# Kernel tuning notes

Measured on AMD Instinct MI355X. Metric: run time of the kernel, lower is better.

The kernel has to match this reference:

```python
import jax, jax.numpy as jnp
import numpy as np

EPS = 1e-5

def layer_norm(x, w, b):
    mu = x.mean(-1, keepdims=True)
    var = x.var(-1, keepdims=True)
    return (x - mu) / jnp.sqrt(var + EPS) * w + b

def s5_forward(u, Lambda_re, Lambda_im, B_re, B_im, C_re, C_im, D, log_step):
    # u: [B, L, H]; diagonal S5 SSM with P complex states, ZOH discretization.
    Lam = (Lambda_re + 1j * Lambda_im).astype(jnp.complex64)          # [P]
    dt = jnp.exp(log_step).astype(jnp.complex64)                       # [P]
    Lam_bar = jnp.exp(Lam * dt)                                        # [P]
    Bc = (B_re + 1j * B_im).astype(jnp.complex64)                      # [P, H]
    B_bar = ((Lam_bar - 1.0) / Lam)[:, None] * Bc                      # [P, H]
    Bu = jnp.einsum('blh,ph->blp', u.astype(jnp.complex64), B_bar)     # [B, L, P]
    A = jnp.broadcast_to(Lam_bar, Bu.shape)                            # [B, L, P]

    def binop(e1, e2):
        a1, b1 = e1
        a2, b2 = e2
        return (a2 * a1, a2 * b1 + b2)

    _, xs = jax.lax.associative_scan(binop, (A, Bu), axis=1)           # [B, L, P]
    Cc = (C_re + 1j * C_im).astype(jnp.complex64)                      # [H, P]
    y = 2.0 * jnp.einsum('blp,hp->blh', xs, Cc).real + D * u           # [B, L, H]
    return y

def setup_inputs() -> dict:
    key = jax.random.key(0)
    ks = jax.random.split(key, 12)
    B, L, H, P = 4, 4096, 512, 512
    x = jax.random.normal(ks[0], (B, L, H), jnp.float32)
    # SSM params (HiPPO-like flavor: negative real part, spread imaginary part)
    Lambda_re = -(0.5 * jax.random.uniform(ks[1], (P,), jnp.float32) + 0.1)
    Lambda_im = jnp.pi * jnp.arange(P, dtype=jnp.float32)
    B_re = jax.random.normal(ks[2], (P, H), jnp.float32) / np.sqrt(2.0 * H)
    B_im = jax.random.normal(ks[3], (P, H), jnp.float32) / np.sqrt(2.0 * H)
    C_re = jax.random.normal(ks[4], (H, P), jnp.float32) / np.sqrt(P)
    C_im = jax.random.normal(ks[5], (H, P), jnp.float32) / np.sqrt(P)
    D = jax.random.normal(ks[6], (H,), jnp.float32)
    log_step = jax.random.uniform(ks[7], (P,), jnp.float32,
                                  minval=np.log(1e-3), maxval=np.log(1e-1))
    ln1_w = jnp.ones((H,), jnp.float32); ln1_b = jnp.zeros((H,), jnp.float32)
    ln2_w = jnp.ones((H,), jnp.float32); ln2_b = jnp.zeros((H,), jnp.float32)
    W_enc = jax.random.normal(ks[8], (2 * H, H), jnp.float32) / np.sqrt(H)
    W_dec = jax.random.normal(ks[9], (H, H), jnp.float32) / np.sqrt(H)
    return {"x": x, "ln1_w": ln1_w, "ln1_b": ln1_b,
            "Lambda_re": Lambda_re, "Lambda_im": Lambda_im,
            "B_re": B_re, "B_im": B_im, "C_re": C_re, "C_im": C_im,
            "D": D, "log_step": log_step,
            "ln2_w": ln2_w, "ln2_b": ln2_b, "W_enc": W_enc, "W_dec": W_dec}

def reference(x, ln1_w, ln1_b, Lambda_re, Lambda_im, B_re, B_im, C_re, C_im,
              D, log_step, ln2_w, ln2_b, W_enc, W_dec):
    fx = layer_norm(x, ln1_w, ln1_b)
    res = fx
    u = s5_forward(fx, Lambda_re, Lambda_im, B_re, B_im, C_re, C_im, D, log_step)
    h = jax.nn.gelu(u, approximate=False) + res  # eval mode: dropout = identity
    fx2 = layer_norm(h, ln2_w, ln2_b)
    e = fx2 @ W_enc.T                              # [B, L, 2H]
    a, g = jnp.split(e, 2, axis=-1)
    ff = a * jax.nn.gelu(g, approximate=False)     # GEGLU
    out = ff @ W_dec.T + fx2
    return out
```

## Files before the change

### kernel.cpp

```cpp
#include <hip/hip_runtime.h>
#include <math.h>

#define Bz 4
#define Lz 4096
#define Hz 512
#define Pz 512
#define Nz (Bz*Lz)
#define CL 64
#define NC (Lz/CL)
#define CS (Bz*NC*Pz)
#define EPSf 1e-5f

typedef unsigned short u16;
typedef unsigned int   u32;
typedef __attribute__((ext_vector_type(8))) short bf16x8;
typedef __attribute__((ext_vector_type(8))) short short8v;
typedef __attribute__((ext_vector_type(4))) short short4v;
typedef __attribute__((ext_vector_type(4))) float f32x4;

__device__ __forceinline__ float gelu_exact(float x){
    return 0.5f * x * (1.0f + erff(x * 0.70710678118654752f));
}
__device__ __forceinline__ u16 f2b(float f){
    union { float f; u32 u; } v; v.f = f;
    u32 u = v.u;
    u32 r = (u + 0x7FFFu + ((u >> 16) & 1u)) >> 16;
    return (u16)r;
}
__device__ __forceinline__ float b2f(u16 h){
    union { u32 u; float f; } v; v.u = ((u32)h) << 16; return v.f;
}

__device__ __forceinline__ void gload_lds16(const u16* g, u16* l){
    __builtin_amdgcn_global_load_lds(
        (const __attribute__((address_space(1))) void*)g,
        (__attribute__((address_space(3))) void*)l, 16, 0, 0);
}

__device__ __forceinline__ void load8(const float* p, float* v){
    f32x4 a = *(const f32x4*)p, c = *(const f32x4*)(p+4);
    #pragma unroll
    for (int j=0;j<4;++j){ v[j]=a[j]; v[4+j]=c[j]; }
}
__device__ __forceinline__ void load8(const u16* p, float* v){
    short8v s = *(const short8v*)p;
    #pragma unroll
    for (int j=0;j<8;++j) v[j] = b2f((u16)s[j]);
}

__global__ void setup_kernel(const float* __restrict__ Lre, const float* __restrict__ Lim,
                             const float* __restrict__ log_step,
                             float* __restrict__ prm){
    int p = blockIdx.x*blockDim.x + threadIdx.x;
    if (p >= Pz) return;
    float lr = Lre[p], li = Lim[p];
    float dt = expf(log_step[p]);
    float ar = lr*dt, ai = li*dt;
    float e = expf(ar);
    float Abr = e*cosf(ai), Abi = e*sinf(ai);
    prm[p]        = Abr;
    prm[Pz + p]   = Abi;
    float nr = Abr - 1.0f, ni = Abi;
    float d2 = lr*lr + li*li;
    prm[2*Pz + p] = (nr*lr + ni*li)/d2;
    prm[3*Pz + p] = (ni*lr - nr*li)/d2;
    float arC = ar*(float)CL, aiC = ai*(float)CL;
    float eC = expf(arC);
    prm[4*Pz + p] = eC*cosf(aiC);
    prm[5*Pz + p] = eC*sinf(aiC);
}

__global__ __launch_bounds__(256) void cvt_all(const float* __restrict__ B_re,
                                               const float* __restrict__ B_im,
                                               const float* __restrict__ C_re,
                                               const float* __restrict__ C_im,
                                               const float* __restrict__ W_enc,
                                               const float* __restrict__ W_dec,
                                               u16* __restrict__ Bcat,
                                               u16* __restrict__ Ccat,
                                               u16* __restrict__ Wenc,
                                               u16* __restrict__ Wdec){
    const int Q = 512*512;
    int i = blockIdx.x*256 + threadIdx.x;
    if (i < Q){ Bcat[i] = f2b(B_re[i]); return; }
    i -= Q;
    if (i < Q){ Bcat[Q + i] = f2b(B_im[i]); return; }
    i -= Q;
    if (i < Q){
        int h = i >> 9, p = i & 511;
        Ccat[(size_t)h*1024 + p]       = f2b(C_re[i]);
        Ccat[(size_t)h*1024 + 512 + p] = f2b(-C_im[i]);
        return;
    }
    i -= Q;
    if (i < 2*Q){ Wenc[i] = f2b(W_enc[i]); return; }
    i -= 2*Q;
    Wdec[i] = f2b(W_dec[i]);
}

template<typename T>
__global__ __launch_bounds__(256) void ln_kernel(const T* __restrict__ in,
                                                 const float* __restrict__ w,
                                                 const float* __restrict__ b,
                                                 u16* __restrict__ ob){
    int row = blockIdx.x*4 + (threadIdx.x >> 6);
    int l = threadIdx.x & 63;
    float v[8];
    load8(in + (size_t)row*Hz + l*8, v);
    float s = 0.f, q = 0.f;
    #pragma unroll
    for (int j=0;j<8;++j){ s += v[j]; q += v[j]*v[j]; }
    #pragma unroll
    for (int o=32;o;o>>=1){ s += __shfl_xor(s,o); q += __shfl_xor(q,o); }
    float mu = s * (1.0f/512.0f);
    float rs = rsqrtf(q * (1.0f/512.0f) - mu*mu + EPSf);
    short8v o8;
    #pragma unroll
    for (int j=0;j<8;++j){
        int m = l*8 + j;
        o8[j] = (short)f2b((v[j]-mu)*rs*w[m] + b[m]);
    }
    *(short8v*)&ob[(size_t)row*Hz + l*8] = o8;
}

#define EB16 0
#define EY   1
#define ERES 2

__device__ __forceinline__ void stage128(const u16* __restrict__ src, int ld,
                                         int grow0, int kt, u16* lds){
    int lane = threadIdx.x & 63;
    int w    = threadIdx.x >> 6;
    #pragma unroll
    for (int q = 0; q < 4; ++q){
        int c = w + q*4;
        int r = c*8 + (lane >> 3);
        int colE = 8*((lane & 7) ^ ((lane >> 3) & 7));
        const u16* g = src + (size_t)(grow0 + r)*ld + kt + colE;
        gload_lds16(g, lds + c*512);
    }
}

template<int K, int EPI>
__global__ __launch_bounds__(256, 2)
void gemm2p(const u16* __restrict__ A, const u16* __restrict__ Bw, int M,
            u16* __restrict__ outB,
            const u16* __restrict__ fxB,
            const float* __restrict__ Dv,
            const u16* __restrict__ resB,
            float* __restrict__ outF)
{
    constexpr int NT = K/64;
    __shared__ u16 AL[2][128*64];
    __shared__ u16 BL[2][128*64];

    int nx = gridDim.x, ny = gridDim.y;
    int nwg = nx*ny;
    int lid = blockIdx.x + blockIdx.y*nx;
    int cpx = nwg >> 3;
    int gdx = (lid & 7)*cpx + (lid >> 3);
    int n0 = (gdx / ny) * 128;
    int m0 = (gdx % ny) * 128;

    int l = threadIdx.x & 63;
    int w = threadIdx.x >> 6;
    int lrow  = l & 15;
    int lcol0 = ((l >> 4)*8) ^ ((l & 7) << 3);
    int lcol1 = lcol0 ^ 32;
    int colw  = w*32;

    f32x4 acc[8][2];
    #pragma unroll
    for (int i=0;i<8;++i){ acc[i][0]=(f32x4)(0.f); acc[i][1]=(f32x4)(0.f); }

    stage128(A,  K, n0, 0, &AL[0][0]);
    stage128(Bw, K, m0, 0, &BL[0][0]);
    __syncthreads();

    for (int T=0; T<NT; ++T){
        int buf = T & 1, nb = buf ^ 1;
        if (T+1 < NT){
            int ktn = (T+1)*64;
            stage128(A,  K, n0, ktn, &AL[nb][0]);
            stage128(Bw, K, m0, ktn, &BL[nb][0]);
        }
        const u16* Ab = &AL[buf][0];
        const u16* Bb = &BL[buf][0];
        bf16x8 bfr[2][2];
        #pragma unroll
        for (int fn=0; fn<2; ++fn){
            bfr[0][fn] = *(const bf16x8*)&Bb[(colw + fn*16 + lrow)*64 + lcol0];
            bfr[1][fn] = *(const bf16x8*)&Bb[(colw + fn*16 + lrow)*64 + lcol1];
        }
        #pragma unroll
        for (int f=0; f<8; ++f){
            bf16x8 a0 = *(const bf16x8*)&Ab[(f*16 + lrow)*64 + lcol0];
            bf16x8 a1 = *(const bf16x8*)&Ab[(f*16 + lrow)*64 + lcol1];
            #pragma unroll
            for (int fn=0; fn<2; ++fn){
                acc[f][fn] = __builtin_amdgcn_mfma_f32_16x16x32_bf16(a0, bfr[0][fn], acc[f][fn], 0,0,0);
                acc[f][fn] = __builtin_amdgcn_mfma_f32_16x16x32_bf16(a1, bfr[1][fn], acc[f][fn], 0,0,0);
            }
        }
        __syncthreads();
    }

    int er = (l >> 4) * 4;
    int ec = l & 15;
    #pragma unroll
    for (int fm=0; fm<8; ++fm)
        #pragma unroll
        for (int fn=0; fn<2; ++fn)
            #pragma unroll
            for (int q=0; q<4; ++q){
                int n = n0 + fm*16 + er + q;
                int m = m0 + colw + fn*16 + ec;
                float v = acc[fm][fn][q];
                if (EPI == EB16){
                    outB[(size_t)n*M + m] = f2b(v);
                } else if (EPI == EY){
                    size_t idx = (size_t)n*Hz + m;
                    float fxv = b2f(fxB[idx]);
                    float y = 2.0f*v + Dv[m]*fxv;
                    outB[idx] = f2b(gelu_exact(y) + fxv);
                } else {
                    size_t idx = (size_t)n*Hz + m;
                    outF[idx] = v + b2f(resB[idx]);
                }
            }
}

__global__ __launch_bounds__(64) void scan_phase1(const u16* __restrict__ g,
                                                  const float* __restrict__ prm,
                                                  float* __restrict__ ERe,
                                                  float* __restrict__ EIm){
    int t = blockIdx.x;
    int ph = t & 1; t >>= 1;
    int c  = t % NC;
    int b  = t / NC;
    int p0 = ph*256 + threadIdx.x*4;
    size_t base = ((size_t)(b*Lz + c*CL))*1024;
    float Ar[4], Ai[4], fr[4], fi[4], xr[4], xi[4];
    #pragma unroll
    for (int j=0;j<4;++j){
        Ar[j]=prm[p0+j]; Ai[j]=prm[Pz+p0+j];
        fr[j]=prm[2*Pz+p0+j]; fi[j]=prm[3*Pz+p0+j];
        xr[j]=0.f; xi[j]=0.f;
    }
    for (int ll=0; ll<CL; ++ll){
        short4v g4 = *(const short4v*)&g[base + p0];
        short4v h4 = *(const short4v*)&g[base + 512 + p0];
        #pragma unroll
        for (int j=0;j<4;++j){
            float gr = b2f((u16)g4[j]), gi = b2f((u16)h4[j]);
            float br = fr[j]*gr - fi[j]*gi;
            float bi = fr[j]*gi + fi[j]*gr;
            float nr = Ar[j]*xr[j] - Ai[j]*xi[j] + br;
            float ni = Ar[j]*xi[j] + Ai[j]*xr[j] + bi;
            xr[j]=nr; xi[j]=ni;
        }
        base += 1024;
    }
    size_t ci = ((size_t)(b*NC + c))*Pz + p0;
    f32x4 er4, ei4;
    #pragma unroll
    for (int j=0;j<4;++j){ er4[j]=xr[j]; ei4[j]=xi[j]; }
    *(f32x4*)&ERe[ci] = er4;
    *(f32x4*)&EIm[ci] = ei4;
}

__global__ __launch_bounds__(256) void scan_combine(const float* __restrict__ ERe,
                                                    const float* __restrict__ EIm,
                                                    const float* __restrict__ prm,
                                                    float* __restrict__ SinRe,
                                                    float* __restrict__ SinIm){
    int gt = blockIdx.x*256 + threadIdx.x;
    int b = gt / Pz, p = gt % Pz;
    float Ar = prm[4*Pz+p], Ai = prm[5*Pz+p];
    float Sr = 0.f, Si = 0.f;
    for (int c = 0; c < NC; ++c) {
        size_t idx = ((size_t)(b*NC + c))*Pz + p;
        SinRe[idx] = Sr; SinIm[idx] = Si;
        float er = ERe[idx], ei = EIm[idx];
        float nr = Ar*Sr - Ai*Si + er;
        float ni = Ar*Si + Ai*Sr + ei;
        Sr = nr; Si = ni;
    }
}

__global__ __launch_bounds__(64) void scan_phase2(u16* __restrict__ g,
                                                  const float* __restrict__ prm,
                                                  const float* __restrict__ SinRe,
                                                  const float* __restrict__ SinIm){
    int t = blockIdx.x;
    int ph = t & 1; t >>= 1;
    int c  = t % NC;
    int b  = t / NC;
    int p0 = ph*256 + threadIdx.x*4;
    size_t base = ((size_t)(b*Lz + c*CL))*1024;
    size_t ci = ((size_t)(b*NC + c))*Pz + p0;
    float Ar[4], Ai[4], fr[4], fi[4], xr[4], xi[4];
    f32x4 sr4 = *(const f32x4*)&SinRe[ci];
    f32x4 si4 = *(const f32x4*)&SinIm[ci];
    #pragma unroll
    for (int j=0;j<4;++j){
        Ar[j]=prm[p0+j]; Ai[j]=prm[Pz+p0+j];
        fr[j]=prm[2*Pz+p0+j]; fi[j]=prm[3*Pz+p0+j];
        xr[j]=sr4[j]; xi[j]=si4[j];
    }
    for (int ll=0; ll<CL; ++ll){
        short4v g4 = *(const short4v*)&g[base + p0];
        short4v h4 = *(const short4v*)&g[base + 512 + p0];
        short4v o4, p4;
        #pragma unroll
        for (int j=0;j<4;++j){
            float gr = b2f((u16)g4[j]), gi = b2f((u16)h4[j]);
            float br = fr[j]*gr - fi[j]*gi;
            float bi = fr[j]*gi + fi[j]*gr;
            float nr = Ar[j]*xr[j] - Ai[j]*xi[j] + br;
            float ni = Ar[j]*xi[j] + Ai[j]*xr[j] + bi;
            xr[j]=nr; xi[j]=ni;
            o4[j] = (short)f2b(nr);
            p4[j] = (short)f2b(ni);
        }
        *(short4v*)&g[base + p0]       = o4;
        *(short4v*)&g[base + 512 + p0] = p4;
        base += 1024;
    }
}

__global__ __launch_bounds__(256) void geglu_kernel(const u16* __restrict__ e,
                                                    u16* __restrict__ ff){
    int i = blockIdx.x*256 + threadIdx.x;
    int n = i >> 6, mc = (i & 63)*8;
    short8v a8 = *(const short8v*)&e[(size_t)n*1024 + mc];
    short8v g8 = *(const short8v*)&e[(size_t)n*1024 + 512 + mc];
    short8v o8;
    #pragma unroll
    for (int j=0;j<8;++j)
        o8[j] = (short)f2b(b2f((u16)a8[j]) * gelu_exact(b2f((u16)g8[j])));
    *(short8v*)&ff[(size_t)n*512 + mc] = o8;
}

extern "C" void kernel_launch(void* const* d_in, const int* in_sizes, int n_in,
                              void* d_out, int out_size, void* d_ws, size_t ws_size,
                              hipStream_t stream) {
    const float* x        = (const float*)d_in[0];
    const float* ln1_w    = (const float*)d_in[1];
    const float* ln1_b    = (const float*)d_in[2];
    const float* Lre      = (const float*)d_in[3];
    const float* Lim      = (const float*)d_in[4];
    const float* B_re     = (const float*)d_in[5];
    const float* B_im     = (const float*)d_in[6];
    const float* C_re     = (const float*)d_in[7];
    const float* C_im     = (const float*)d_in[8];
    const float* Dv       = (const float*)d_in[9];
    const float* log_step = (const float*)d_in[10];
    const float* ln2_w    = (const float*)d_in[11];
    const float* ln2_b    = (const float*)d_in[12];
    const float* W_enc    = (const float*)d_in[13];
    const float* W_dec    = (const float*)d_in[14];
    float* out = (float*)d_out;

    const size_t NH = (size_t)Nz*Hz;
    char* W = (char*)d_ws;
    u16*   fxb  = (u16*)  (W);
    u16*   g    = (u16*)  (W + NH*2);
    u16*   hb   = (u16*)  (W + NH*6);
    u16*   fx2b = (u16*)  (W + NH*8);
    float* ERe  = (float*)(W + NH*10);
    float* EIm  = ERe + CS;
    float* SinRe= EIm + CS;
    float* SinIm= SinRe + CS;
    float* prm  = SinIm + CS;
    u16*   Bcat = (u16*)(prm + 6*Pz);
    u16*   Ccat = Bcat + 1024*512;
    u16*   Wenc = Ccat + 512*1024;
    u16*   Wdec = Wenc + 1024*512;

    setup_kernel<<<dim3(2), dim3(256), 0, stream>>>(Lre, Lim, log_step, prm);

    cvt_all<<<dim3(6*1024), dim3(256), 0, stream>>>(B_re, B_im, C_re, C_im, W_enc, W_dec,
                                                    Bcat, Ccat, Wenc, Wdec);

    ln_kernel<float><<<dim3(Nz/4), dim3(256), 0, stream>>>(x, ln1_w, ln1_b, fxb);

    gemm2p<512,EB16><<<dim3(Nz/128, 1024/128), dim3(256), 0, stream>>>(
        fxb, Bcat, 1024, g, nullptr, nullptr, nullptr, nullptr);

    scan_phase1<<<dim3(Bz*NC*2), dim3(64), 0, stream>>>(g, prm, ERe, EIm);
    scan_combine<<<dim3((Bz*Pz)/256), dim3(256), 0, stream>>>(ERe, EIm, prm, SinRe, SinIm);
    scan_phase2<<<dim3(Bz*NC*2), dim3(64), 0, stream>>>(g, prm, SinRe, SinIm);

    gemm2p<1024,EY><<<dim3(Nz/128, 512/128), dim3(256), 0, stream>>>(
        g, Ccat, 512, hb, fxb, Dv, nullptr, nullptr);

    ln_kernel<u16><<<dim3(Nz/4), dim3(256), 0, stream>>>(hb, ln2_w, ln2_b, fx2b);

    gemm2p<512,EB16><<<dim3(Nz/128, 1024/128), dim3(256), 0, stream>>>(
        fx2b, Wenc, 1024, g, nullptr, nullptr, nullptr, nullptr);

    geglu_kernel<<<dim3(Nz*64/256), dim3(256), 0, stream>>>(g, fxb);

    gemm2p<512,ERES><<<dim3(Nz/128, 512/128), dim3(256), 0, stream>>>(
        fxb, Wdec, 512, nullptr, nullptr, nullptr, fx2b, out);
}
```

Measured before the change: 189.7 us.

## Fuse scan phase1 into B-projection GEMM and GEGLU into encoder GEMM

```diff
diff --git a/kernel.cpp b/kernel.cpp
--- a/kernel.cpp
+++ b/kernel.cpp
@@ -15,7 +15,6 @@
 typedef unsigned int   u32;
 typedef __attribute__((ext_vector_type(8))) short bf16x8;
 typedef __attribute__((ext_vector_type(8))) short short8v;
-typedef __attribute__((ext_vector_type(4))) short short4v;
 typedef __attribute__((ext_vector_type(4))) float f32x4;
 
 __device__ __forceinline__ float gelu_exact(float x){
@@ -82,14 +81,14 @@
                                                u16* __restrict__ Wdec){
     const int Q = 512*512;
     int i = blockIdx.x*256 + threadIdx.x;
-    if (i < Q){ Bcat[i] = f2b(B_re[i]); return; }
+    if (i < Q){ int p=i>>9, h=i&511; Bcat[(size_t)(2*p)*512 + h]   = f2b(B_re[i]); return; }
     i -= Q;
-    if (i < Q){ Bcat[Q + i] = f2b(B_im[i]); return; }
+    if (i < Q){ int p=i>>9, h=i&511; Bcat[(size_t)(2*p+1)*512 + h] = f2b(B_im[i]); return; }
     i -= Q;
     if (i < Q){
         int h = i >> 9, p = i & 511;
-        Ccat[(size_t)h*1024 + p]       = f2b(C_re[i]);
-        Ccat[(size_t)h*1024 + 512 + p] = f2b(-C_im[i]);
+        Ccat[(size_t)h*1024 + 2*p]     = f2b(C_re[i]);
+        Ccat[(size_t)h*1024 + 2*p + 1] = f2b(-C_im[i]);
         return;
     }
     i -= Q;
@@ -230,43 +229,196 @@
             }
 }
 
-__global__ __launch_bounds__(64) void scan_phase1(const u16* __restrict__ g,
-                                                  const float* __restrict__ prm,
-                                                  float* __restrict__ ERe,
-                                                  float* __restrict__ EIm){
-    int t = blockIdx.x;
-    int ph = t & 1; t >>= 1;
-    int c  = t % NC;
-    int b  = t / NC;
-    int p0 = ph*256 + threadIdx.x*4;
-    size_t base = ((size_t)(b*Lz + c*CL))*1024;
-    float Ar[4], Ai[4], fr[4], fi[4], xr[4], xi[4];
-    #pragma unroll
-    for (int j=0;j<4;++j){
-        Ar[j]=prm[p0+j]; Ai[j]=prm[Pz+p0+j];
-        fr[j]=prm[2*Pz+p0+j]; fi[j]=prm[3*Pz+p0+j];
-        xr[j]=0.f; xi[j]=0.f;
-    }
-    for (int ll=0; ll<CL; ++ll){
-        short4v g4 = *(const short4v*)&g[base + p0];
-        short4v h4 = *(const short4v*)&g[base + 512 + p0];
-        #pragma unroll
-        for (int j=0;j<4;++j){
-            float gr = b2f((u16)g4[j]), gi = b2f((u16)h4[j]);
-            float br = fr[j]*gr - fi[j]*gi;
-            float bi = fr[j]*gi + fi[j]*gr;
-            float nr = Ar[j]*xr[j] - Ai[j]*xi[j] + br;
-            float ni = Ar[j]*xi[j] + Ai[j]*xr[j] + bi;
-            xr[j]=nr; xi[j]=ni;
-        }
-        base += 1024;
-    }
-    size_t ci = ((size_t)(b*NC + c))*Pz + p0;
-    f32x4 er4, ei4;
-    #pragma unroll
-    for (int j=0;j<4;++j){ er4[j]=xr[j]; ei4[j]=xi[j]; }
-    *(f32x4*)&ERe[ci] = er4;
-    *(f32x4*)&EIm[ci] = ei4;
+__global__ __launch_bounds__(256, 2)
+void gemm1_scan(const u16* __restrict__ A, const u16* __restrict__ Bw,
+                u16* __restrict__ outB,
+                const float* __restrict__ prm,
+                float* __restrict__ ERe, float* __restrict__ EIm)
+{
+    constexpr int K = 512, NT = K/64;
+    __shared__ u16 AL[2][128*64];
+    __shared__ u16 BL[2][128*64];
+
+    int nx = gridDim.x, ny = gridDim.y;
+    int nwg = nx*ny;
+    int lid = blockIdx.x + blockIdx.y*nx;
+    int cpx = nwg >> 3;
+    int gdx = (lid & 7)*cpx + (lid >> 3);
+    int n0 = (gdx / ny) * 128;
+    int m0 = (gdx % ny) * 128;
+
+    int l = threadIdx.x & 63;
+    int w = threadIdx.x >> 6;
+    int lrow  = l & 15;
+    int lcol0 = ((l >> 4)*8) ^ ((l & 7) << 3);
+    int lcol1 = lcol0 ^ 32;
+    int colw  = w*32;
+
+    f32x4 acc[8][2];
+    #pragma unroll
+    for (int i=0;i<8;++i){ acc[i][0]=(f32x4)(0.f); acc[i][1]=(f32x4)(0.f); }
+
+    stage128(A,  K, n0, 0, &AL[0][0]);
+    stage128(Bw, K, m0, 0, &BL[0][0]);
+    __syncthreads();
+
+    for (int T=0; T<NT; ++T){
+        int buf = T & 1, nb = buf ^ 1;
+        if (T+1 < NT){
+            int ktn = (T+1)*64;
+            stage128(A,  K, n0, ktn, &AL[nb][0]);
+            stage128(Bw, K, m0, ktn, &BL[nb][0]);
+        }
+        const u16* Ab = &AL[buf][0];
+        const u16* Bb = &BL[buf][0];
+        bf16x8 bfr[2][2];
+        #pragma unroll
+        for (int fn=0; fn<2; ++fn){
+            bfr[0][fn] = *(const bf16x8*)&Bb[(colw + fn*16 + lrow)*64 + lcol0];
+            bfr[1][fn] = *(const bf16x8*)&Bb[(colw + fn*16 + lrow)*64 + lcol1];
+        }
+        #pragma unroll
+        for (int f=0; f<8; ++f){
+            bf16x8 a0 = *(const bf16x8*)&Ab[(f*16 + lrow)*64 + lcol0];
+            bf16x8 a1 = *(const bf16x8*)&Ab[(f*16 + lrow)*64 + lcol1];
+            #pragma unroll
+            for (int fn=0; fn<2; ++fn){
+                acc[f][fn] = __builtin_amdgcn_mfma_f32_16x16x32_bf16(a0, bfr[0][fn], acc[f][fn], 0,0,0);
+                acc[f][fn] = __builtin_amdgcn_mfma_f32_16x16x32_bf16(a1, bfr[1][fn], acc[f][fn], 0,0,0);
+            }
+        }
+        __syncthreads();
+    }
+
+    u16* gt = (u16*)AL;
+    int er = (l >> 4) * 4;
+    int ec = l & 15;
+    #pragma unroll
+    for (int fm=0; fm<8; ++fm)
+        #pragma unroll
+        for (int fn=0; fn<2; ++fn)
+            #pragma unroll
+            for (int q=0; q<4; ++q){
+                int rr = fm*16 + er + q;
+                int cc = colw + fn*16 + ec;
+                u16 hv = f2b(acc[fm][fn][q]);
+                outB[(size_t)(n0 + rr)*1024 + (m0 + cc)] = hv;
+                gt[rr*128 + cc] = hv;
+            }
+    __syncthreads();
+
+    int tid = threadIdx.x;
+    if (tid < 128){
+        int p = tid & 63, h = tid >> 6;
+        int P = (m0 >> 1) + p;
+        int b = n0 >> 12;
+        int c = ((n0 & 4095) >> 6) + h;
+        float Ar = prm[P], Ai = prm[Pz+P];
+        float fre = prm[2*Pz+P], fim = prm[3*Pz+P];
+        float xr = 0.f, xi = 0.f;
+        int base = h*64*128 + 2*p;
+        #pragma unroll 8
+        for (int r = 0; r < 64; ++r){
+            u32 v = *(const u32*)&gt[base + r*128];
+            float gr = b2f((u16)(v & 0xffff));
+            float gi = b2f((u16)(v >> 16));
+            float br = fre*gr - fim*gi;
+            float bi = fre*gi + fim*gr;
+            float nr2 = Ar*xr - Ai*xi + br;
+            float ni2 = Ar*xi + Ai*xr + bi;
+            xr = nr2; xi = ni2;
+        }
+        size_t ci = ((size_t)(b*NC + c))*Pz + P;
+        ERe[ci] = xr; EIm[ci] = xi;
+    }
+}
+
+__device__ __forceinline__ void stageWglu(const u16* __restrict__ src, int m0,
+                                          int kt, u16* lds){
+    int lane = threadIdx.x & 63;
+    int w    = threadIdx.x >> 6;
+    #pragma unroll
+    for (int q = 0; q < 4; ++q){
+        int c = w + q*4;
+        int r = c*8 + (lane >> 3);
+        int rb = r >> 4;
+        int grow = (rb & 1) ? (512 + m0 + ((rb>>1)<<4) + (r & 15))
+                            : (      m0 + ((rb>>1)<<4) + (r & 15));
+        int colE = 8*((lane & 7) ^ ((lane >> 3) & 7));
+        gload_lds16(src + (size_t)grow*512 + kt + colE, lds + c*512);
+    }
+}
+
+__global__ __launch_bounds__(256, 2)
+void gemm3glu(const u16* __restrict__ A, const u16* __restrict__ Wenc,
+              u16* __restrict__ outB)
+{
+    constexpr int K = 512, NT = K/64;
+    __shared__ u16 AL[2][128*64];
+    __shared__ u16 BL[2][128*64];
+
+    int nx = gridDim.x, ny = gridDim.y;
+    int nwg = nx*ny;
+    int lid = blockIdx.x + blockIdx.y*nx;
+    int cpx = nwg >> 3;
+    int gdx = (lid & 7)*cpx + (lid >> 3);
+    int n0 = (gdx / ny) * 128;
+    int m0 = (gdx % ny) * 64;
+
+    int l = threadIdx.x & 63;
+    int w = threadIdx.x >> 6;
+    int lrow  = l & 15;
+    int lcol0 = ((l >> 4)*8) ^ ((l & 7) << 3);
+    int lcol1 = lcol0 ^ 32;
+    int colw  = w*32;
+
+    f32x4 acc[8][2];
+    #pragma unroll
+    for (int i=0;i<8;++i){ acc[i][0]=(f32x4)(0.f); acc[i][1]=(f32x4)(0.f); }
+
+    stage128(A, K, n0, 0, &AL[0][0]);
+    stageWglu(Wenc, m0, 0, &BL[0][0]);
+    __syncthreads();
+
+    for (int T=0; T<NT; ++T){
+        int buf = T & 1, nb = buf ^ 1;
+        if (T+1 < NT){
+            int ktn = (T+1)*64;
+            stage128(A, K, n0, ktn, &AL[nb][0]);
+            stageWglu(Wenc, m0, ktn, &BL[nb][0]);
+        }
+        const u16* Ab = &AL[buf][0];
+        const u16* Bb = &BL[buf][0];
+        bf16x8 bfr[2][2];
+        #pragma unroll
+        for (int fn=0; fn<2; ++fn){
+            bfr[0][fn] = *(const bf16x8*)&Bb[(colw + fn*16 + lrow)*64 + lcol0];
+            bfr[1][fn] = *(const bf16x8*)&Bb[(colw + fn*16 + lrow)*64 + lcol1];
+        }
+        #pragma unroll
+        for (int f=0; f<8; ++f){
+            bf16x8 a0 = *(const bf16x8*)&Ab[(f*16 + lrow)*64 + lcol0];
+            bf16x8 a1 = *(const bf16x8*)&Ab[(f*16 + lrow)*64 + lcol1];
+            #pragma unroll
+            for (int fn=0; fn<2; ++fn){
+                acc[f][fn] = __builtin_amdgcn_mfma_f32_16x16x32_bf16(a0, bfr[0][fn], acc[f][fn], 0,0,0);
+                acc[f][fn] = __builtin_amdgcn_mfma_f32_16x16x32_bf16(a1, bfr[1][fn], acc[f][fn], 0,0,0);
+            }
+        }
+        __syncthreads();
+    }
+
+    int er = (l >> 4) * 4;
+    int ec = l & 15;
+    int col = m0 + w*16 + ec;
+    #pragma unroll
+    for (int fm=0; fm<8; ++fm)
+        #pragma unroll
+        for (int q=0; q<4; ++q){
+            int n = n0 + fm*16 + er + q;
+            float ffv = acc[fm][0][q] * gelu_exact(acc[fm][1][q]);
+            outB[(size_t)n*Hz + col] = f2b(ffv);
+        }
 }
 
 __global__ __launch_bounds__(256) void scan_combine(const float* __restrict__ ERe,
@@ -297,6 +449,7 @@
     int c  = t % NC;
     int b  = t / NC;
     int p0 = ph*256 + threadIdx.x*4;
+    int cb = 2*p0;
     size_t base = ((size_t)(b*Lz + c*CL))*1024;
     size_t ci = ((size_t)(b*NC + c))*Pz + p0;
     float Ar[4], Ai[4], fr[4], fi[4], xr[4], xi[4];
@@ -309,37 +462,22 @@
         xr[j]=sr4[j]; xi[j]=si4[j];
     }
     for (int ll=0; ll<CL; ++ll){
-        short4v g4 = *(const short4v*)&g[base + p0];
-        short4v h4 = *(const short4v*)&g[base + 512 + p0];
-        short4v o4, p4;
+        short8v v8 = *(const short8v*)&g[base + cb];
+        short8v o8;
         #pragma unroll
         for (int j=0;j<4;++j){
-            float gr = b2f((u16)g4[j]), gi = b2f((u16)h4[j]);
+            float gr = b2f((u16)v8[2*j]), gi = b2f((u16)v8[2*j+1]);
             float br = fr[j]*gr - fi[j]*gi;
             float bi = fr[j]*gi + fi[j]*gr;
             float nr = Ar[j]*xr[j] - Ai[j]*xi[j] + br;
             float ni = Ar[j]*xi[j] + Ai[j]*xr[j] + bi;
             xr[j]=nr; xi[j]=ni;
-            o4[j] = (short)f2b(nr);
-            p4[j] = (short)f2b(ni);
-        }
-        *(short4v*)&g[base + p0]       = o4;
-        *(short4v*)&g[base + 512 + p0] = p4;
+            o8[2*j]   = (short)f2b(nr);
+            o8[2*j+1] = (short)f2b(ni);
+        }
+        *(short8v*)&g[base + cb] = o8;
         base += 1024;
     }
-}
-
-__global__ __launch_bounds__(256) void geglu_kernel(const u16* __restrict__ e,
-                                                    u16* __restrict__ ff){
-    int i = blockIdx.x*256 + threadIdx.x;
-    int n = i >> 6, mc = (i & 63)*8;
-    short8v a8 = *(const short8v*)&e[(size_t)n*1024 + mc];
-    short8v g8 = *(const short8v*)&e[(size_t)n*1024 + 512 + mc];
-    short8v o8;
-    #pragma unroll
-    for (int j=0;j<8;++j)
-        o8[j] = (short)f2b(b2f((u16)a8[j]) * gelu_exact(b2f((u16)g8[j])));
-    *(short8v*)&ff[(size_t)n*512 + mc] = o8;
 }
 
 extern "C" void kernel_launch(void* const* d_in, const int* in_sizes, int n_in,
@@ -385,10 +523,9 @@
 
     ln_kernel<float><<<dim3(Nz/4), dim3(256), 0, stream>>>(x, ln1_w, ln1_b, fxb);
 
-    gemm2p<512,EB16><<<dim3(Nz/128, 1024/128), dim3(256), 0, stream>>>(
-        fxb, Bcat, 1024, g, nullptr, nullptr, nullptr, nullptr);
-
-    scan_phase1<<<dim3(Bz*NC*2), dim3(64), 0, stream>>>(g, prm, ERe, EIm);
+    gemm1_scan<<<dim3(Nz/128, 1024/128), dim3(256), 0, stream>>>(
+        fxb, Bcat, g, prm, ERe, EIm);
+
     scan_combine<<<dim3((Bz*Pz)/256), dim3(256), 0, stream>>>(ERe, EIm, prm, SinRe, SinIm);
     scan_phase2<<<dim3(Bz*NC*2), dim3(64), 0, stream>>>(g, prm, SinRe, SinIm);
 
@@ -397,10 +534,7 @@
 
     ln_kernel<u16><<<dim3(Nz/4), dim3(256), 0, stream>>>(hb, ln2_w, ln2_b, fx2b);
 
-    gemm2p<512,EB16><<<dim3(Nz/128, 1024/128), dim3(256), 0, stream>>>(
-        fx2b, Wenc, 1024, g, nullptr, nullptr, nullptr, nullptr);
-
-    geglu_kernel<<<dim3(Nz*64/256), dim3(256), 0, stream>>>(g, fxb);
+    gemm3glu<<<dim3(Nz/128, 8), dim3(256), 0, stream>>>(fx2b, Wenc, fxb);
 
     gemm2p<512,ERES><<<dim3(Nz/128, 512/128), dim3(256), 0, stream>>>(
         fxb, Wdec, 512, nullptr, nullptr, nullptr, fx2b, out);
```

Result: faster. 185.6 us (-2.1%).
